# Kernel optimization log

Measured on AMD Instinct MI355X. Metric: run time of the kernel, lower is better.

The kernel has to match this reference:

```python
import jax, jax.numpy as jnp
import numpy as np


def _dependence(X):
    # X: [N, D]. dom[i, j] = True iff X[i, d] > X[j, d] for all d.
    # Diagonal is automatically False (X[i] > X[i] is all False), matching the
    # original's explicit i != j exclusion.
    dom = jnp.all(X[:, None, :] > X[None, :, :], axis=-1)  # [N, N] bool
    n = X.shape[0]
    Z = dom.sum(axis=1).astype(X.dtype) / (n - 1)  # [N]
    return Z


def setup_inputs() -> dict:
    key = jax.random.key(0)
    k1, k2 = jax.random.split(key)
    N, D = 8192, 8
    X = jax.random.normal(k1, (N, D), dtype=jnp.float32)
    X_hat = jax.random.normal(k2, (N, D), dtype=jnp.float32)
    return {"X": X, "X_hat": X_hat}


def reference(X, X_hat):
    Z = jnp.sort(_dependence(X))
    Zhat = jnp.sort(_dependence(X_hat))
    return jnp.sum(jnp.abs(Z - Zhat)) / Z.shape[0]
```

## Files before the change

### kernel.cpp

```cpp
#include <hip/hip_runtime.h>

constexpr int N = 8192;
constexpr int BLK = 256;
constexpr int IPT = 4;
constexpr int ITILE = BLK * IPT;
constexpr int JTILE = 256;
constexpr int JCH = N / JTILE;

__device__ __forceinline__ float min3f(float a, float b, float c) {
  float r;
  asm("v_min3_f32 %0, %1, %2, %3" : "=v"(r) : "v"(a), "v"(b), "v"(c));
  return r;
}
__device__ __forceinline__ float min2f(float a, float b) {
  float r;
  asm("v_min_f32 %0, %1, %2" : "=v"(r) : "v"(a), "v"(b));
  return r;
}

__global__ __launch_bounds__(BLK) void dom_count_kernel(
    const float* __restrict__ X, const float* __restrict__ Xh,
    int* __restrict__ counts) {
  const float* M = (blockIdx.z == 0) ? X : Xh;
  int* cnt_out = counts + blockIdx.z * N;

  __shared__ float4 tile[JTILE * 2];

  const int tid = threadIdx.x;
  const int ibase = blockIdx.x * ITILE + tid;

  const int j0 = blockIdx.y * JTILE;
  const float4* src = reinterpret_cast<const float4*>(M + (size_t)j0 * 8);
  for (int k = tid; k < JTILE * 2; k += BLK) tile[k] = src[k];

  float4 r0[IPT], r1[IPT];
#pragma unroll
  for (int p = 0; p < IPT; ++p) {
    const float4* Mi = reinterpret_cast<const float4*>(M + (size_t)(ibase + p * BLK) * 8);
    r0[p] = Mi[0];
    r1[p] = Mi[1];
  }
  __syncthreads();

  int cnt[IPT] = {};
#pragma unroll 2
  for (int j = 0; j < JTILE; ++j) {
    const float4 a = tile[2 * j];
    const float4 b = tile[2 * j + 1];
#pragma unroll
    for (int p = 0; p < IPT; ++p) {
      const float t0 = min3f(r0[p].x - a.x, r0[p].y - a.y, r0[p].z - a.z);
      const float t1 = min3f(r0[p].w - a.w, r1[p].x - b.x, r1[p].y - b.y);
      const float t2 = min2f(r1[p].z - b.z, r1[p].w - b.w);
      cnt[p] += (min3f(t0, t1, t2) > 0.0f) ? 1 : 0;
    }
  }
#pragma unroll
  for (int p = 0; p < IPT; ++p) atomicAdd(&cnt_out[ibase + p * BLK], cnt[p]);
}

constexpr int HB = 16;
__global__ __launch_bounds__(1024) void hist_partial_kernel(
    const int* __restrict__ counts, int* __restrict__ ghist) {
  __shared__ int lhist[N];
  const int tid = threadIdx.x;
  for (int q = tid; q < N; q += 1024) lhist[q] = 0;
  __syncthreads();

  const int k = blockIdx.x * (2 * N / HB) + tid;
  const int v = counts[k];
  atomicAdd(&lhist[v], (k < N) ? 1 : -1);
  __syncthreads();

#pragma unroll
  for (int q = 0; q < N / 1024; ++q) {
    const int bin = tid * (N / 1024) + q;
    const int h = lhist[bin];
    if (h != 0) atomicAdd(&ghist[bin], h);
  }
}

__global__ __launch_bounds__(1024) void finalize_kernel(
    const int* __restrict__ ghist, float* __restrict__ out) {
  __shared__ int wsum[16];
  __shared__ int wexc[16];
  __shared__ int wabs[16];

  const int tid = threadIdx.x;
  const int lane = tid & 63;
  const int wid = tid >> 6;

  int local[8];
  int s = 0;
#pragma unroll
  for (int q = 0; q < 8; ++q) {
    local[q] = ghist[tid * 8 + q];
    s += local[q];
  }

  int incl = s;
#pragma unroll
  for (int off = 1; off < 64; off <<= 1) {
    const int v = __shfl_up(incl, off);
    if (lane >= off) incl += v;
  }
  if (lane == 63) wsum[wid] = incl;
  __syncthreads();

  if (tid == 0) {
    int acc = 0;
#pragma unroll
    for (int w = 0; w < 16; ++w) { wexc[w] = acc; acc += wsum[w]; }
  }
  __syncthreads();

  int run = wexc[wid] + (incl - s);
  int acc = 0;
#pragma unroll
  for (int q = 0; q < 8; ++q) {
    run += local[q];
    acc += (run < 0) ? -run : run;
  }

#pragma unroll
  for (int off = 32; off > 0; off >>= 1) acc += __shfl_down(acc, off);
  if (lane == 0) wabs[wid] = acc;
  __syncthreads();

  if (tid == 0) {
    int total = 0;
#pragma unroll
    for (int w = 0; w < 16; ++w) total += wabs[w];
    out[0] = (float)((double)total / ((double)(N - 1) * (double)N));
  }
}

extern "C" void kernel_launch(void* const* d_in, const int* in_sizes, int n_in,
                              void* d_out, int out_size, void* d_ws, size_t ws_size,
                              hipStream_t stream) {
  const float* X = (const float*)d_in[0];
  const float* Xh = (const float*)d_in[1];
  float* out = (float*)d_out;
  int* counts = (int*)d_ws;
  int* ghist = counts + 2 * N;

  hipMemsetAsync(counts, 0, (2 * N + N) * sizeof(int), stream);

  dim3 grid(N / ITILE, JCH, 2);
  dom_count_kernel<<<grid, BLK, 0, stream>>>(X, Xh, counts);
  hist_partial_kernel<<<HB, 1024, 0, stream>>>(counts, ghist);
  finalize_kernel<<<1, 1024, 0, stream>>>(ghist, out);
}
```

Baseline: 104.7 us.

## Fuse memset, dominance, histogram and finalize into one cooperative kernel

Replaces the memset plus three launches with a single cooperative-groups kernel that separates the phases with grid-wide syncs, removing per-launch overhead. The dominance tile is retiled (IPT 8, JTILE 128, 512 units, one per block). The compare now stores negated tile values so packed v_pk_add_f32 produces two differences per instruction. The histogram is split into radix ranges across 32 blocks. It keeps a non-cooperative fallback path and adds grid.sync costs and a dependence on co-residency of 512 blocks.

```diff
diff --git a/kernel.cpp b/kernel.cpp
--- a/kernel.cpp
+++ b/kernel.cpp
@@ -1,12 +1,27 @@
 #include <hip/hip_runtime.h>
+#include <hip/hip_cooperative_groups.h>
+
+namespace cg = cooperative_groups;
 
 constexpr int N = 8192;
 constexpr int BLK = 256;
-constexpr int IPT = 4;
+constexpr int IPT = 8;
 constexpr int ITILE = BLK * IPT;
-constexpr int JTILE = 256;
+constexpr int NIT = N / ITILE;
+constexpr int JTILE = 128;
 constexpr int JCH = N / JTILE;
-
+constexpr int UNITS = NIT * JCH * 2;
+constexpr int COOP_GRID = 512;
+constexpr int HB = 32;
+
+typedef float f32x2 __attribute__((ext_vector_type(2)));
+typedef float f32x4 __attribute__((ext_vector_type(4)));
+
+__device__ __forceinline__ f32x2 pk_add(f32x2 a, f32x2 b) {
+  f32x2 r;
+  asm("v_pk_add_f32 %0, %1, %2" : "=v"(r) : "v"(a), "v"(b));
+  return r;
+}
 __device__ __forceinline__ float min3f(float a, float b, float c) {
   float r;
   asm("v_min3_f32 %0, %1, %2, %3" : "=v"(r) : "v"(a), "v"(b), "v"(c));
@@ -17,26 +32,34 @@
   asm("v_min_f32 %0, %1, %2" : "=v"(r) : "v"(a), "v"(b));
   return r;
 }
-
-__global__ __launch_bounds__(BLK) void dom_count_kernel(
-    const float* __restrict__ X, const float* __restrict__ Xh,
-    int* __restrict__ counts) {
-  const float* M = (blockIdx.z == 0) ? X : Xh;
-  int* cnt_out = counts + blockIdx.z * N;
-
-  __shared__ float4 tile[JTILE * 2];
-
-  const int tid = threadIdx.x;
-  const int ibase = blockIdx.x * ITILE + tid;
-
-  const int j0 = blockIdx.y * JTILE;
-  const float4* src = reinterpret_cast<const float4*>(M + (size_t)j0 * 8);
-  for (int k = tid; k < JTILE * 2; k += BLK) tile[k] = src[k];
-
-  float4 r0[IPT], r1[IPT];
+__device__ __forceinline__ int aload(const int* p) {
+  return __hip_atomic_load(p, __ATOMIC_RELAXED, __HIP_MEMORY_SCOPE_AGENT);
+}
+__device__ __forceinline__ void astore(int* p, int v) {
+  __hip_atomic_store(p, v, __ATOMIC_RELAXED, __HIP_MEMORY_SCOPE_AGENT);
+}
+
+__device__ __forceinline__ void dom_unit(int u, const float* __restrict__ X,
+                                         const float* __restrict__ Xh,
+                                         int* __restrict__ counts,
+                                         f32x4* tile) {
+  const int tid = threadIdx.x;
+  const int m = u & 1;
+  const int b2 = u >> 1;
+  const int it = b2 & (NIT - 1);
+  const int jc = b2 >> 2;
+  const float* __restrict__ M = m ? Xh : X;
+  int* cnt_out = counts + m * N;
+
+  __syncthreads();
+  const f32x4* src = reinterpret_cast<const f32x4*>(M + (size_t)(jc * JTILE) * 8);
+  tile[tid] = -src[tid];
+
+  const int ibase = it * ITILE + tid;
+  f32x4 r0[IPT], r1[IPT];
 #pragma unroll
   for (int p = 0; p < IPT; ++p) {
-    const float4* Mi = reinterpret_cast<const float4*>(M + (size_t)(ibase + p * BLK) * 8);
+    const f32x4* Mi = reinterpret_cast<const f32x4*>(M + (size_t)(ibase + p * BLK) * 8);
     r0[p] = Mi[0];
     r1[p] = Mi[1];
   }
@@ -45,56 +68,57 @@
   int cnt[IPT] = {};
 #pragma unroll 2
   for (int j = 0; j < JTILE; ++j) {
-    const float4 a = tile[2 * j];
-    const float4 b = tile[2 * j + 1];
+    const f32x4 a = tile[2 * j];
+    const f32x4 b = tile[2 * j + 1];
 #pragma unroll
     for (int p = 0; p < IPT; ++p) {
-      const float t0 = min3f(r0[p].x - a.x, r0[p].y - a.y, r0[p].z - a.z);
-      const float t1 = min3f(r0[p].w - a.w, r1[p].x - b.x, r1[p].y - b.y);
-      const float t2 = min2f(r1[p].z - b.z, r1[p].w - b.w);
-      cnt[p] += (min3f(t0, t1, t2) > 0.0f) ? 1 : 0;
+      const f32x2 d01 = pk_add(r0[p].xy, a.xy);
+      const f32x2 d23 = pk_add(r0[p].zw, a.zw);
+      const f32x2 d45 = pk_add(r1[p].xy, b.xy);
+      const f32x2 d67 = pk_add(r1[p].zw, b.zw);
+      const float t0 = min3f(d01.x, d01.y, d23.x);
+      const float t1 = min3f(d23.y, d45.x, d45.y);
+      const float t2 = min3f(d67.x, d67.y, t0);
+      cnt[p] += (min2f(t1, t2) > 0.0f) ? 1 : 0;
     }
   }
 #pragma unroll
   for (int p = 0; p < IPT; ++p) atomicAdd(&cnt_out[ibase + p * BLK], cnt[p]);
 }
 
-constexpr int HB = 16;
-__global__ __launch_bounds__(1024) void hist_partial_kernel(
-    const int* __restrict__ counts, int* __restrict__ ghist) {
-  __shared__ int lhist[N];
-  const int tid = threadIdx.x;
-  for (int q = tid; q < N; q += 1024) lhist[q] = 0;
-  __syncthreads();
-
-  const int k = blockIdx.x * (2 * N / HB) + tid;
-  const int v = counts[k];
-  atomicAdd(&lhist[v], (k < N) ? 1 : -1);
-  __syncthreads();
-
-#pragma unroll
-  for (int q = 0; q < N / 1024; ++q) {
-    const int bin = tid * (N / 1024) + q;
-    const int h = lhist[bin];
-    if (h != 0) atomicAdd(&ghist[bin], h);
-  }
-}
-
-__global__ __launch_bounds__(1024) void finalize_kernel(
-    const int* __restrict__ ghist, float* __restrict__ out) {
-  __shared__ int wsum[16];
-  __shared__ int wexc[16];
-  __shared__ int wabs[16];
-
+__device__ __forceinline__ void hist_block(int hb, const int* __restrict__ counts,
+                                           int* __restrict__ ghist, int* lhist) {
+  const int tid = threadIdx.x;
+  const int rg = hb & 3;
+  const int sl = hb >> 2;
+  __syncthreads();
+  for (int q = tid; q < 2048; q += BLK) lhist[q] = 0;
+  __syncthreads();
+#pragma unroll
+  for (int t = 0; t < 2048 / BLK; ++t) {
+    const int k = sl * 2048 + t * BLK + tid;
+    const int v = aload(&counts[k]);
+    if ((v >> 11) == rg) atomicAdd(&lhist[v & 2047], (k < N) ? 1 : -1);
+  }
+  __syncthreads();
+  for (int q = tid; q < 2048; q += BLK) {
+    const int h = lhist[q];
+    if (h != 0) atomicAdd(&ghist[rg * 2048 + q], h);
+  }
+}
+
+__device__ __forceinline__ void fin_block(const int* __restrict__ ghist,
+                                          float* __restrict__ out, int* fin) {
   const int tid = threadIdx.x;
   const int lane = tid & 63;
   const int wid = tid >> 6;
-
-  int local[8];
+  __syncthreads();
+
+  int local[32];
   int s = 0;
 #pragma unroll
-  for (int q = 0; q < 8; ++q) {
-    local[q] = ghist[tid * 8 + q];
+  for (int q = 0; q < 32; ++q) {
+    local[q] = aload(&ghist[tid * 32 + q]);
     s += local[q];
   }
 
@@ -104,35 +128,72 @@
     const int v = __shfl_up(incl, off);
     if (lane >= off) incl += v;
   }
-  if (lane == 63) wsum[wid] = incl;
-  __syncthreads();
-
+  if (lane == 63) fin[wid] = incl;
+  __syncthreads();
   if (tid == 0) {
     int acc = 0;
 #pragma unroll
-    for (int w = 0; w < 16; ++w) { wexc[w] = acc; acc += wsum[w]; }
-  }
-  __syncthreads();
-
-  int run = wexc[wid] + (incl - s);
+    for (int w = 0; w < 4; ++w) { const int t = fin[w]; fin[4 + w] = acc; acc += t; }
+  }
+  __syncthreads();
+
+  int run = fin[4 + wid] + (incl - s);
   int acc = 0;
 #pragma unroll
-  for (int q = 0; q < 8; ++q) {
+  for (int q = 0; q < 32; ++q) {
     run += local[q];
     acc += (run < 0) ? -run : run;
   }
-
 #pragma unroll
   for (int off = 32; off > 0; off >>= 1) acc += __shfl_down(acc, off);
-  if (lane == 0) wabs[wid] = acc;
-  __syncthreads();
-
+  if (lane == 0) fin[8 + wid] = acc;
+  __syncthreads();
   if (tid == 0) {
-    int total = 0;
-#pragma unroll
-    for (int w = 0; w < 16; ++w) total += wabs[w];
+    const int total = fin[8] + fin[9] + fin[10] + fin[11];
     out[0] = (float)((double)total / ((double)(N - 1) * (double)N));
   }
+}
+
+__global__ __launch_bounds__(BLK, 2) void kendall_coop(
+    const float* __restrict__ X, const float* __restrict__ Xh,
+    int* __restrict__ counts,
+    int* __restrict__ ghist,
+    float* __restrict__ out) {
+  cg::grid_group g = cg::this_grid();
+  __shared__ union {
+    f32x4 tile[JTILE * 2];
+    int lhist[2048];
+    int fin[16];
+  } smem;
+  const int bid = blockIdx.x;
+  const int tid = threadIdx.x;
+
+  for (int k = bid * BLK + tid; k < 3 * N; k += COOP_GRID * BLK) astore(&counts[k], 0);
+  g.sync();
+
+  dom_unit(bid, X, Xh, counts, smem.tile);
+  g.sync();
+
+  if (bid < HB) hist_block(bid, counts, ghist, smem.lhist);
+  g.sync();
+
+  if (bid == 0) fin_block(ghist, out, smem.fin);
+}
+
+__global__ __launch_bounds__(BLK) void dom_kernel_fb(
+    const float* __restrict__ X, const float* __restrict__ Xh, int* __restrict__ counts) {
+  __shared__ f32x4 tile[JTILE * 2];
+  dom_unit(blockIdx.x, X, Xh, counts, tile);
+}
+__global__ __launch_bounds__(BLK) void hist_kernel_fb(
+    const int* __restrict__ counts, int* __restrict__ ghist) {
+  __shared__ int lhist[2048];
+  hist_block(blockIdx.x, counts, ghist, lhist);
+}
+__global__ __launch_bounds__(BLK) void fin_kernel_fb(
+    const int* __restrict__ ghist, float* __restrict__ out) {
+  __shared__ int fin[16];
+  fin_block(ghist, out, fin);
 }
 
 extern "C" void kernel_launch(void* const* d_in, const int* in_sizes, int n_in,
@@ -144,10 +205,14 @@
   int* counts = (int*)d_ws;
   int* ghist = counts + 2 * N;
 
-  hipMemsetAsync(counts, 0, (2 * N + N) * sizeof(int), stream);
-
-  dim3 grid(N / ITILE, JCH, 2);
-  dom_count_kernel<<<grid, BLK, 0, stream>>>(X, Xh, counts);
-  hist_partial_kernel<<<HB, 1024, 0, stream>>>(counts, ghist);
-  finalize_kernel<<<1, 1024, 0, stream>>>(ghist, out);
-}
+  void* args[5] = {(void*)&X, (void*)&Xh, (void*)&counts, (void*)&ghist, (void*)&out};
+  const hipError_t err = hipLaunchCooperativeKernel(
+      (void*)kendall_coop, dim3(COOP_GRID), dim3(BLK), args, 0, stream);
+
+  if (err != hipSuccess) {
+    hipMemsetAsync(counts, 0, 3 * N * sizeof(int), stream);
+    dom_kernel_fb<<<UNITS, BLK, 0, stream>>>(X, Xh, counts);
+    hist_kernel_fb<<<HB, BLK, 0, stream>>>(counts, ghist);
+    fin_kernel_fb<<<1, BLK, 0, stream>>>(ghist, out);
+  }
+}
```

Measured after the change: 245.5 us. 2.35x slower.

## Use scalar-loaded j rows and v_cmpx exec-masking chain for dominance count

Applied to the files above, without the earlier changes.

Replaces the LDS-tiled min3 reduction with a per-thread loop where the j rows are fetched through scalar loads (s_load_dwordx16) into SGPRs. Each dominance test becomes a chain of eight v_cmpx_lt_f32 instructions that narrow the exec mask, an add, and an exec restore. This removes the subtract, min and compare work, the LDS traffic and the barrier. In exchange it drops register blocking to one i per thread, raises grid size, relies on hand-written exec manipulation in inline asm, and leaves scalar-load latency exposed by waiting on lgkmcnt each iteration.

```diff
diff --git a/kernel.cpp b/kernel.cpp
--- a/kernel.cpp
+++ b/kernel.cpp
@@ -2,61 +2,74 @@
 
 constexpr int N = 8192;
 constexpr int BLK = 256;
-constexpr int IPT = 4;
-constexpr int ITILE = BLK * IPT;
-constexpr int JTILE = 256;
-constexpr int JCH = N / JTILE;
+constexpr int JSPLIT = 32;
+constexpr int JSEG = N / JSPLIT;
 
-__device__ __forceinline__ float min3f(float a, float b, float c) {
-  float r;
-  asm("v_min3_f32 %0, %1, %2, %3" : "=v"(r) : "v"(a), "v"(b), "v"(c));
-  return r;
-}
-__device__ __forceinline__ float min2f(float a, float b) {
-  float r;
-  asm("v_min_f32 %0, %1, %2" : "=v"(r) : "v"(a), "v"(b));
-  return r;
-}
+typedef float f32x4 __attribute__((ext_vector_type(4)));
+typedef uint32_t u32x16 __attribute__((ext_vector_type(16)));
 
-__global__ __launch_bounds__(BLK) void dom_count_kernel(
+#define SLOAD16(dst, base, immstr) \
+  asm volatile("s_load_dwordx16 %0, %1, " immstr : "=s"(dst) : "s"(base))
+
+#define DOMSTEP(r, k0)                                                       \
+  asm volatile(                                                              \
+      "v_cmpx_lt_f32 vcc, %[a0], %[x0]\n\t"                                  \
+      "v_cmpx_lt_f32 vcc, %[a1], %[x1]\n\t"                                  \
+      "v_cmpx_lt_f32 vcc, %[a2], %[x2]\n\t"                                  \
+      "v_cmpx_lt_f32 vcc, %[a3], %[x3]\n\t"                                  \
+      "v_cmpx_lt_f32 vcc, %[a4], %[x4]\n\t"                                  \
+      "v_cmpx_lt_f32 vcc, %[a5], %[x5]\n\t"                                  \
+      "v_cmpx_lt_f32 vcc, %[a6], %[x6]\n\t"                                  \
+      "v_cmpx_lt_f32 vcc, %[a7], %[x7]\n\t"                                  \
+      "v_add_u32 %[c], 1, %[c]\n\t"                                          \
+      "s_mov_b64 exec, %[sv]"                                                \
+      : [c] "+v"(cnt)                                                        \
+      : [a0] "s"(r[k0 + 0]), [a1] "s"(r[k0 + 1]), [a2] "s"(r[k0 + 2]),       \
+        [a3] "s"(r[k0 + 3]), [a4] "s"(r[k0 + 4]), [a5] "s"(r[k0 + 5]),       \
+        [a6] "s"(r[k0 + 6]), [a7] "s"(r[k0 + 7]), [x0] "v"(xi0),             \
+        [x1] "v"(xi1), [x2] "v"(xi2), [x3] "v"(xi3), [x4] "v"(xi4),          \
+        [x5] "v"(xi5), [x6] "v"(xi6), [x7] "v"(xi7), [sv] "s"(sv)            \
+      : "vcc")
+
+__global__ __launch_bounds__(BLK, 4) void dom_count_kernel(
     const float* __restrict__ X, const float* __restrict__ Xh,
     int* __restrict__ counts) {
-  const float* M = (blockIdx.z == 0) ? X : Xh;
+  const float* __restrict__ M = (blockIdx.z == 0) ? X : Xh;
   int* cnt_out = counts + blockIdx.z * N;
 
-  __shared__ float4 tile[JTILE * 2];
+  const int i = blockIdx.x * BLK + threadIdx.x;
 
-  const int tid = threadIdx.x;
-  const int ibase = blockIdx.x * ITILE + tid;
+  const f32x4* Mi = reinterpret_cast<const f32x4*>(M + (size_t)i * 8);
+  const f32x4 ra = Mi[0];
+  const f32x4 rb = Mi[1];
+  const float xi0 = ra.x, xi1 = ra.y, xi2 = ra.z, xi3 = ra.w;
+  const float xi4 = rb.x, xi5 = rb.y, xi6 = rb.z, xi7 = rb.w;
 
-  const int j0 = blockIdx.y * JTILE;
-  const float4* src = reinterpret_cast<const float4*>(M + (size_t)j0 * 8);
-  for (int k = tid; k < JTILE * 2; k += BLK) tile[k] = src[k];
+  uint64_t sv;
+  asm volatile("s_mov_b64 %0, exec" : "=s"(sv));
 
-  float4 r0[IPT], r1[IPT];
-#pragma unroll
-  for (int p = 0; p < IPT; ++p) {
-    const float4* Mi = reinterpret_cast<const float4*>(M + (size_t)(ibase + p * BLK) * 8);
-    r0[p] = Mi[0];
-    r1[p] = Mi[1];
+  int cnt = 0;
+  const float* jb = M + (size_t)(blockIdx.y * JSEG) * 8;
+  for (int jj = 0; jj < JSEG; jj += 8) {
+    u32x16 q0, q1, q2, q3;
+    const float* gb = jb + (size_t)jj * 8;
+    SLOAD16(q0, gb, "0x0");
+    SLOAD16(q1, gb, "0x40");
+    SLOAD16(q2, gb, "0x80");
+    SLOAD16(q3, gb, "0xC0");
+    asm volatile("s_waitcnt lgkmcnt(0)"
+                 : "+s"(q0), "+s"(q1), "+s"(q2), "+s"(q3));
+    DOMSTEP(q0, 0);
+    DOMSTEP(q0, 8);
+    DOMSTEP(q1, 0);
+    DOMSTEP(q1, 8);
+    DOMSTEP(q2, 0);
+    DOMSTEP(q2, 8);
+    DOMSTEP(q3, 0);
+    DOMSTEP(q3, 8);
   }
-  __syncthreads();
 
-  int cnt[IPT] = {};
-#pragma unroll 2
-  for (int j = 0; j < JTILE; ++j) {
-    const float4 a = tile[2 * j];
-    const float4 b = tile[2 * j + 1];
-#pragma unroll
-    for (int p = 0; p < IPT; ++p) {
-      const float t0 = min3f(r0[p].x - a.x, r0[p].y - a.y, r0[p].z - a.z);
-      const float t1 = min3f(r0[p].w - a.w, r1[p].x - b.x, r1[p].y - b.y);
-      const float t2 = min2f(r1[p].z - b.z, r1[p].w - b.w);
-      cnt[p] += (min3f(t0, t1, t2) > 0.0f) ? 1 : 0;
-    }
-  }
-#pragma unroll
-  for (int p = 0; p < IPT; ++p) atomicAdd(&cnt_out[ibase + p * BLK], cnt[p]);
+  atomicAdd(&cnt_out[i], cnt);
 }
 
 constexpr int HB = 16;
@@ -144,9 +157,9 @@
   int* counts = (int*)d_ws;
   int* ghist = counts + 2 * N;
 
-  hipMemsetAsync(counts, 0, (2 * N + N) * sizeof(int), stream);
+  hipMemsetAsync(counts, 0, 3 * N * sizeof(int), stream);
 
-  dim3 grid(N / ITILE, JCH, 2);
+  dim3 grid(N / BLK, JSPLIT, 2);
   dom_count_kernel<<<grid, BLK, 0, stream>>>(X, Xh, counts);
   hist_partial_kernel<<<HB, 1024, 0, stream>>>(counts, ghist);
   finalize_kernel<<<1, 1024, 0, stream>>>(ghist, out);
```

Measured after the change: 104.3 us. Within noise of the previous version (-0.4%).
